# Kernel tuning notes

Measured on AMD Instinct MI355X. Metric: run time of the kernel, lower is better.

Reference implementation:

```python
import jax, jax.numpy as jnp
import numpy as np

D_MODEL = 128
REDUCTION = 4
KSIZE = 3
B = D_MODEL  # required by the original code's groups=B conv shape constraint
L = 4096


def setup_inputs() -> dict:
    key = jax.random.key(0)
    ks = jax.random.split(key, 7)
    d, r, K = D_MODEL, REDUCTION, KSIZE
    return {
        "x": jax.random.normal(ks[0], (B, L, d), dtype=jnp.float32),
        "W1": jax.random.normal(ks[1], (d // r, d), dtype=jnp.float32) * (1.0 / np.sqrt(d)),
        "b1": jax.random.normal(ks[2], (d // r,), dtype=jnp.float32) * 0.01,
        "W2": jax.random.normal(ks[3], (K, d // r), dtype=jnp.float32) * (1.0 / np.sqrt(d // r)),
        "b2": jax.random.normal(ks[4], (K,), dtype=jnp.float32) * 0.01,
        "Wc": jax.random.normal(ks[5], (d, d), dtype=jnp.float32) * (1.0 / np.sqrt(d)),
        "bc": jax.random.normal(ks[6], (d,), dtype=jnp.float32) * 0.01,
    }


def reference(x, W1, b1, W2, b2, Wc, bc):
    # x: [B, L, d] with B == d (required by original groups=B conv)
    Bsz, Lseq, d = x.shape
    K = W2.shape[0]
    pad = (K - 1) // 2
    # kernel generation from global average pool
    m = x.mean(axis=1)                                   # [B, d]
    h = jax.nn.gelu(m @ W1.T + b1, approximate=False)    # [B, d//r]
    w = jax.nn.softmax(h @ W2.T + b2, axis=-1)           # [B, K]; row j is the kernel for channel j
    # depthwise-style cross-correlation: y[b, l, c] = sum_k xp[b, l+k, c] * w[c, k]
    xp = jnp.pad(x, ((0, 0), (pad, pad), (0, 0)))        # [B, L+2*pad, d]
    y = sum(xp[:, k:k + Lseq, :] * w[None, None, :, k] for k in range(K))  # [B, L, d]
    # pointwise conv (kernel_size=1) == per-token linear
    return y @ Wc.T + bc                                 # [B, L, d]
```

## Files before the change

### kernel.cpp

```cpp
#include <hip/hip_runtime.h>
#include <hip/hip_bf16.h>

#define D_MODEL 128
#define SEQ_L   4096
#define BATCH   128
#define NSEG    8

typedef float f4 __attribute__((ext_vector_type(4)));
typedef float f32x4 __attribute__((ext_vector_type(4)));
typedef short bf16x8 __attribute__((ext_vector_type(8)));

__device__ __forceinline__ unsigned short f2bf(float f) {
    union { float f; unsigned u; } v; v.f = f;
    unsigned r = v.u + 0x7FFFu + ((v.u >> 16) & 1u);
    return (unsigned short)(r >> 16);
}

__global__ __launch_bounds__(512) void kmean(const float* __restrict__ x,
                                             float* __restrict__ part,
                                             const float* __restrict__ Wc,
                                             unsigned short* __restrict__ wcb) {
    if (blockIdx.x == NSEG) {
        if (blockIdx.y < 8) {
            int i = blockIdx.y * 512 + threadIdx.x;
            f4 v = reinterpret_cast<const f4*>(Wc)[i];
            ushort4 o;
            o.x = f2bf(v[0]); o.y = f2bf(v[1]); o.z = f2bf(v[2]); o.w = f2bf(v[3]);
            reinterpret_cast<ushort4*>(wcb)[i] = o;
        }
        return;
    }
    int seg = blockIdx.x, b = blockIdx.y;
    int t = threadIdx.x;
    int c4 = t & 31, ph = t >> 5;
    const f4* xb = reinterpret_cast<const f4*>(x + (size_t)b * SEQ_L * D_MODEL);
    int l0 = seg * (SEQ_L / NSEG);

    f4 a0 = {0.f,0.f,0.f,0.f}, a1 = a0, a2 = a0, a3 = a0;
    #pragma unroll
    for (int i = 0; i < 32; i += 4) {
        a0 += xb[(l0 + ph + (i + 0) * 16) * 32 + c4];
        a1 += xb[(l0 + ph + (i + 1) * 16) * 32 + c4];
        a2 += xb[(l0 + ph + (i + 2) * 16) * 32 + c4];
        a3 += xb[(l0 + ph + (i + 3) * 16) * 32 + c4];
    }
    f4 acc = (a0 + a1) + (a2 + a3);

    __shared__ f4 red[512];
    red[t] = acc;
    __syncthreads();
    if (t < 32) {
        f4 s = red[t];
        #pragma unroll
        for (int p = 1; p < 16; ++p) s += red[t + 32 * p];
        reinterpret_cast<f4*>(part + ((size_t)b * NSEG + seg) * D_MODEL)[t] = s;
    }
}

__global__ __launch_bounds__(128) void kweights(const float* __restrict__ part,
                                                const float* __restrict__ W1,
                                                const float* __restrict__ b1,
                                                const float* __restrict__ W2,
                                                const float* __restrict__ b2,
                                                float* __restrict__ w) {
    int c = threadIdx.x;
    f4 mv[32];
    #pragma unroll
    for (int d4 = 0; d4 < 32; ++d4) mv[d4] = (f4){0.f, 0.f, 0.f, 0.f};
    for (int s = 0; s < NSEG; ++s) {
        const f4* ps = reinterpret_cast<const f4*>(part + ((size_t)c * NSEG + s) * D_MODEL);
        #pragma unroll
        for (int d4 = 0; d4 < 32; ++d4) mv[d4] += ps[d4];
    }
    #pragma unroll
    for (int d4 = 0; d4 < 32; ++d4) mv[d4] *= (1.0f / (float)SEQ_L);

    float h[32];
    #pragma unroll
    for (int j = 0; j < 32; ++j) {
        const f4* w1r = reinterpret_cast<const f4*>(W1 + j * 128);
        f4 s4 = {0.f, 0.f, 0.f, 0.f};
        #pragma unroll
        for (int d4 = 0; d4 < 32; ++d4) s4 += mv[d4] * w1r[d4];
        float s = s4[0] + s4[1] + s4[2] + s4[3] + b1[j];
        h[j] = 0.5f * s * (1.0f + erff(s * 0.70710678118654752f));
    }
    float lg[3];
    float mx = -1e30f;
    #pragma unroll
    for (int k = 0; k < 3; ++k) {
        float s = b2[k];
        #pragma unroll
        for (int j = 0; j < 32; ++j) s += h[j] * W2[k * 32 + j];
        lg[k] = s;
        mx = fmaxf(mx, s);
    }
    float e[3], den = 0.f;
    #pragma unroll
    for (int k = 0; k < 3; ++k) { e[k] = __expf(lg[k] - mx); den += e[k]; }
    float inv = 1.0f / den;
    #pragma unroll
    for (int k = 0; k < 3; ++k) w[k * 128 + c] = e[k] * inv;
}

template<bool GUARD>
__device__ __forceinline__ void load6(const float* __restrict__ xb, int gr0, int c4, f4 R[6]) {
    #pragma unroll
    for (int j = 0; j < 6; ++j) {
        int gr = gr0 + j;
        if (GUARD) {
            bool ok = (gr >= 0) && (gr < SEQ_L);
            int grc = ok ? gr : 0;
            f4 v = reinterpret_cast<const f4*>(xb + (size_t)grc * D_MODEL)[c4];
            f4 z = {0.f, 0.f, 0.f, 0.f};
            R[j] = ok ? v : z;
        } else {
            R[j] = reinterpret_cast<const f4*>(xb + (size_t)gr * D_MODEL)[c4];
        }
    }
}

__global__ __launch_bounds__(512, 2) void kconv(const float* __restrict__ x,
                                                const float* __restrict__ wv,
                                                const unsigned short* __restrict__ wcb,
                                                const float* __restrict__ bc,
                                                float* __restrict__ out) {
    __shared__ __align__(16) unsigned short y_lds[2][64][132];

    int t = threadIdx.x;
    int b = blockIdx.y;
    int base = blockIdx.x * 256;
    const float* xb = x + (size_t)b * SEQ_L * D_MODEL;
    float* outb = out + (size_t)b * SEQ_L * D_MODEL;

    int c4 = t & 31, rg = t >> 5;
    int lane = t & 63, wid = t >> 6;
    int r = lane & 15, q = lane >> 4, kb = q * 8;
    int co0 = wid * 16;

    f4 w0 = reinterpret_cast<const f4*>(wv)[c4];
    f4 w1 = reinterpret_cast<const f4*>(wv + 128)[c4];
    f4 w2 = reinterpret_cast<const f4*>(wv + 256)[c4];

    bf16x8 awc[4];
    #pragma unroll
    for (int kc = 0; kc < 4; ++kc)
        awc[kc] = *reinterpret_cast<const bf16x8*>(wcb + (size_t)(co0 + r) * D_MODEL + kc * 32 + kb);

    f4 bcv = *reinterpret_cast<const f4*>(bc + co0 + q * 4);

    f4 R[6];
    if (base == 0) load6<true>(xb, base + rg * 4 - 1, c4, R);
    else           load6<false>(xb, base + rg * 4 - 1, c4, R);

    #pragma unroll
    for (int i = 0; i < 4; ++i) {
        int buf = i & 1;
        #pragma unroll
        for (int j = 0; j < 4; ++j) {
            f4 y = R[j] * w0 + R[j + 1] * w1 + R[j + 2] * w2;
            ushort4 yb;
            yb.x = f2bf(y[0]); yb.y = f2bf(y[1]); yb.z = f2bf(y[2]); yb.w = f2bf(y[3]);
            *reinterpret_cast<ushort4*>(&y_lds[buf][rg * 4 + j][c4 * 4]) = yb;
        }
        if (i < 3) {
            int ntok0 = base + (i + 1) * 64;
            if (ntok0 + 64 == SEQ_L) load6<true>(xb, ntok0 + rg * 4 - 1, c4, R);
            else                     load6<false>(xb, ntok0 + rg * 4 - 1, c4, R);
        }
        __syncthreads();

        f32x4 acc[4];
        #pragma unroll
        for (int g = 0; g < 4; ++g) acc[g] = (f32x4){0.f, 0.f, 0.f, 0.f};
        #pragma unroll
        for (int g = 0; g < 4; ++g)
            #pragma unroll
            for (int kc = 0; kc < 4; ++kc) {
                bf16x8 bv = *reinterpret_cast<const bf16x8*>(&y_lds[buf][g * 16 + r][kc * 32 + kb]);
                acc[g] = __builtin_amdgcn_mfma_f32_16x16x32_bf16(awc[kc], bv, acc[g], 0, 0, 0);
            }

        int tokt = base + i * 64;
        #pragma unroll
        for (int g = 0; g < 4; ++g) {
            int tok = tokt + g * 16 + r;
            *reinterpret_cast<f4*>(outb + (size_t)tok * D_MODEL + co0 + q * 4) = acc[g] + bcv;
        }
        __syncthreads();
    }
}

extern "C" void kernel_launch(void* const* d_in, const int* in_sizes, int n_in,
                              void* d_out, int out_size, void* d_ws, size_t ws_size,
                              hipStream_t stream) {
    const float* x  = (const float*)d_in[0];
    const float* W1 = (const float*)d_in[1];
    const float* b1 = (const float*)d_in[2];
    const float* W2 = (const float*)d_in[3];
    const float* b2 = (const float*)d_in[4];
    const float* Wc = (const float*)d_in[5];
    const float* bc = (const float*)d_in[6];
    float* out = (float*)d_out;

    char* ws = (char*)d_ws;
    float* part = (float*)ws;
    float* w    = (float*)(ws + 524288);
    unsigned short* wcb = (unsigned short*)(ws + 526336);

    kmean<<<dim3(NSEG + 1, BATCH), 512, 0, stream>>>(x, part, Wc, wcb);
    kweights<<<1, 128, 0, stream>>>(part, W1, b1, W2, b2, w);
    kconv<<<dim3(SEQ_L / 256, BATCH), 512, 0, stream>>>(x, w, wcb, bc, out);
}
```

Baseline: 235.7 us.

## Emit bf16 copy of x during mean pass and feed conv from it

The mean-reduction kernel now also writes a bf16 copy of x to workspace. The conv kernel reads that half-size copy instead of the fp32 input, and uses a swizzled LDS layout, 128-token chunks and higher occupancy bounds. The aim is to halve the conv kernel's input read traffic, at the cost of an extra bf16 write in the first pass and reduced precision on the conv input. A fallback keeps the original path when the workspace is too small.

```diff
diff --git a/kernel.cpp b/kernel.cpp
--- a/kernel.cpp
+++ b/kernel.cpp
@@ -9,6 +9,7 @@
 typedef float f4 __attribute__((ext_vector_type(4)));
 typedef float f32x4 __attribute__((ext_vector_type(4)));
 typedef short bf16x8 __attribute__((ext_vector_type(8)));
+typedef unsigned int u32x4 __attribute__((ext_vector_type(4)));
 
 __device__ __forceinline__ unsigned short f2bf(float f) {
     union { float f; unsigned u; } v; v.f = f;
@@ -16,10 +17,27 @@
     return (unsigned short)(r >> 16);
 }
 
-__global__ __launch_bounds__(512) void kmean(const float* __restrict__ x,
-                                             float* __restrict__ part,
-                                             const float* __restrict__ Wc,
-                                             unsigned short* __restrict__ wcb) {
+__device__ __forceinline__ unsigned pack2bf(float lo, float hi) {
+    return (unsigned)f2bf(lo) | ((unsigned)f2bf(hi) << 16);
+}
+
+__device__ __forceinline__ void unpk(u32x4 v, f4& a, f4& b) {
+    a[0] = __uint_as_float(v.x << 16);
+    a[1] = __uint_as_float(v.x & 0xFFFF0000u);
+    a[2] = __uint_as_float(v.y << 16);
+    a[3] = __uint_as_float(v.y & 0xFFFF0000u);
+    b[0] = __uint_as_float(v.z << 16);
+    b[1] = __uint_as_float(v.z & 0xFFFF0000u);
+    b[2] = __uint_as_float(v.w << 16);
+    b[3] = __uint_as_float(v.w & 0xFFFF0000u);
+}
+
+
+__global__ __launch_bounds__(512) void kmean_a(const float* __restrict__ x,
+                                               float* __restrict__ part,
+                                               const float* __restrict__ Wc,
+                                               unsigned short* __restrict__ wcb,
+                                               unsigned short* __restrict__ xbf) {
     if (blockIdx.x == NSEG) {
         if (blockIdx.y < 8) {
             int i = blockIdx.y * 512 + threadIdx.x;
@@ -34,6 +52,161 @@
     int t = threadIdx.x;
     int c4 = t & 31, ph = t >> 5;
     const f4* xb = reinterpret_cast<const f4*>(x + (size_t)b * SEQ_L * D_MODEL);
+    unsigned short* xbb = xbf + (size_t)b * SEQ_L * D_MODEL;
+    int l0 = seg * (SEQ_L / NSEG);
+
+    f4 a0 = {0.f,0.f,0.f,0.f}, a1 = a0, a2 = a0, a3 = a0;
+    #pragma unroll
+    for (int i = 0; i < 32; i += 4) {
+        #pragma unroll
+        for (int k = 0; k < 4; ++k) {
+            int l = l0 + ph + (i + k) * 16;
+            f4 v = xb[l * 32 + c4];
+            if (k == 0) a0 += v; else if (k == 1) a1 += v; else if (k == 2) a2 += v; else a3 += v;
+            ushort4 o;
+            o.x = f2bf(v[0]); o.y = f2bf(v[1]); o.z = f2bf(v[2]); o.w = f2bf(v[3]);
+            reinterpret_cast<ushort4*>(xbb + (size_t)l * D_MODEL)[c4] = o;
+        }
+    }
+    f4 acc = (a0 + a1) + (a2 + a3);
+
+    __shared__ f4 red[512];
+    red[t] = acc;
+    __syncthreads();
+    if (t < 32) {
+        f4 s = red[t];
+        #pragma unroll
+        for (int p = 1; p < 16; ++p) s += red[t + 32 * p];
+        reinterpret_cast<f4*>(part + ((size_t)b * NSEG + seg) * D_MODEL)[t] = s;
+    }
+}
+
+template<bool GUARD>
+__device__ __forceinline__ void load6b(const unsigned short* __restrict__ xbb,
+                                       int gr0, int c8, u32x4 R[6]) {
+    #pragma unroll
+    for (int j = 0; j < 6; ++j) {
+        int gr = gr0 + j;
+        if (GUARD) {
+            bool ok = (gr >= 0) && (gr < SEQ_L);
+            int grc = ok ? gr : 0;
+            u32x4 v = reinterpret_cast<const u32x4*>(xbb + (size_t)grc * D_MODEL)[c8];
+            u32x4 z = {0u, 0u, 0u, 0u};
+            R[j] = ok ? v : z;
+        } else {
+            R[j] = reinterpret_cast<const u32x4*>(xbb + (size_t)gr * D_MODEL)[c8];
+        }
+    }
+}
+
+template<bool GUARD>
+__device__ __forceinline__ void kconv_body(const unsigned short* __restrict__ xbf,
+                                           const float* __restrict__ wv,
+                                           const unsigned short* __restrict__ wcb,
+                                           const float* __restrict__ bc,
+                                           float* __restrict__ out,
+                                           unsigned short (*y_lds)[128][128]) {
+    int t = threadIdx.x, b = blockIdx.y;
+    int base = blockIdx.x * 256;
+    const unsigned short* xbb = xbf + (size_t)b * SEQ_L * D_MODEL;
+    float* outb = out + (size_t)b * SEQ_L * D_MODEL;
+
+    int c8 = t & 15, rg = t >> 4;
+    int lane = t & 63, wid = t >> 6;
+    int r = lane & 15, q = lane >> 4, kb = q * 8;
+    int co0 = wid * 16;
+
+    f4 w0a = *reinterpret_cast<const f4*>(wv + c8 * 8);
+    f4 w0b = *reinterpret_cast<const f4*>(wv + c8 * 8 + 4);
+    f4 w1a = *reinterpret_cast<const f4*>(wv + 128 + c8 * 8);
+    f4 w1b = *reinterpret_cast<const f4*>(wv + 128 + c8 * 8 + 4);
+    f4 w2a = *reinterpret_cast<const f4*>(wv + 256 + c8 * 8);
+    f4 w2b = *reinterpret_cast<const f4*>(wv + 256 + c8 * 8 + 4);
+
+    bf16x8 awc[4];
+    #pragma unroll
+    for (int kc = 0; kc < 4; ++kc)
+        awc[kc] = *reinterpret_cast<const bf16x8*>(wcb + (size_t)(co0 + r) * D_MODEL + kc * 32 + kb);
+
+    f4 bcv = *reinterpret_cast<const f4*>(bc + co0 + q * 4);
+
+    u32x4 R[6];
+    load6b<GUARD>(xbb, base + rg * 4 - 1, c8, R);
+
+    #pragma unroll
+    for (int i = 0; i < 2; ++i) {
+        f4 pa, pb, ca, cb;
+        unpk(R[0], pa, pb);
+        unpk(R[1], ca, cb);
+        #pragma unroll
+        for (int j = 0; j < 4; ++j) {
+            f4 na, nb;
+            unpk(R[j + 2], na, nb);
+            f4 y0 = pa * w0a + ca * w1a + na * w2a;
+            f4 y1 = pb * w0b + cb * w1b + nb * w2b;
+            u32x4 P;
+            P.x = pack2bf(y0[0], y0[1]);
+            P.y = pack2bf(y0[2], y0[3]);
+            P.z = pack2bf(y1[0], y1[1]);
+            P.w = pack2bf(y1[2], y1[3]);
+            int row = rg * 4 + j;
+            *reinterpret_cast<u32x4*>(&y_lds[i][row][(c8 ^ (row & 15)) * 8]) = P;
+            pa = ca; pb = cb; ca = na; cb = nb;
+        }
+        if (i == 0) load6b<GUARD>(xbb, base + 128 + rg * 4 - 1, c8, R);
+        __syncthreads();
+
+        f32x4 acc[8];
+        #pragma unroll
+        for (int g = 0; g < 8; ++g) acc[g] = (f32x4){0.f, 0.f, 0.f, 0.f};
+        #pragma unroll
+        for (int g = 0; g < 8; ++g)
+            #pragma unroll
+            for (int kc = 0; kc < 4; ++kc) {
+                bf16x8 bv = *reinterpret_cast<const bf16x8*>(
+                    &y_lds[i][g * 16 + r][((kc * 4 + q) ^ r) * 8]);
+                acc[g] = __builtin_amdgcn_mfma_f32_16x16x32_bf16(awc[kc], bv, acc[g], 0, 0, 0);
+            }
+
+        #pragma unroll
+        for (int g = 0; g < 8; ++g) {
+            int tok = base + i * 128 + g * 16 + r;
+            *reinterpret_cast<f4*>(outb + (size_t)tok * D_MODEL + co0 + q * 4) = acc[g] + bcv;
+        }
+    }
+}
+
+__global__ __launch_bounds__(512, 4) void kconv_a(const unsigned short* __restrict__ xbf,
+                                                  const float* __restrict__ wv,
+                                                  const unsigned short* __restrict__ wcb,
+                                                  const float* __restrict__ bc,
+                                                  float* __restrict__ out) {
+    __shared__ __align__(16) unsigned short y_lds[2][128][128];
+    if (blockIdx.x == 0 || blockIdx.x == gridDim.x - 1)
+        kconv_body<true>(xbf, wv, wcb, bc, out, y_lds);
+    else
+        kconv_body<false>(xbf, wv, wcb, bc, out, y_lds);
+}
+
+
+__global__ __launch_bounds__(512) void kmean_b(const float* __restrict__ x,
+                                               float* __restrict__ part,
+                                               const float* __restrict__ Wc,
+                                               unsigned short* __restrict__ wcb) {
+    if (blockIdx.x == NSEG) {
+        if (blockIdx.y < 8) {
+            int i = blockIdx.y * 512 + threadIdx.x;
+            f4 v = reinterpret_cast<const f4*>(Wc)[i];
+            ushort4 o;
+            o.x = f2bf(v[0]); o.y = f2bf(v[1]); o.z = f2bf(v[2]); o.w = f2bf(v[3]);
+            reinterpret_cast<ushort4*>(wcb)[i] = o;
+        }
+        return;
+    }
+    int seg = blockIdx.x, b = blockIdx.y;
+    int t = threadIdx.x;
+    int c4 = t & 31, ph = t >> 5;
+    const f4* xb = reinterpret_cast<const f4*>(x + (size_t)b * SEQ_L * D_MODEL);
     int l0 = seg * (SEQ_L / NSEG);
 
     f4 a0 = {0.f,0.f,0.f,0.f}, a1 = a0, a2 = a0, a3 = a0;
@@ -55,52 +228,6 @@
         for (int p = 1; p < 16; ++p) s += red[t + 32 * p];
         reinterpret_cast<f4*>(part + ((size_t)b * NSEG + seg) * D_MODEL)[t] = s;
     }
-}
-
-__global__ __launch_bounds__(128) void kweights(const float* __restrict__ part,
-                                                const float* __restrict__ W1,
-                                                const float* __restrict__ b1,
-                                                const float* __restrict__ W2,
-                                                const float* __restrict__ b2,
-                                                float* __restrict__ w) {
-    int c = threadIdx.x;
-    f4 mv[32];
-    #pragma unroll
-    for (int d4 = 0; d4 < 32; ++d4) mv[d4] = (f4){0.f, 0.f, 0.f, 0.f};
-    for (int s = 0; s < NSEG; ++s) {
-        const f4* ps = reinterpret_cast<const f4*>(part + ((size_t)c * NSEG + s) * D_MODEL);
-        #pragma unroll
-        for (int d4 = 0; d4 < 32; ++d4) mv[d4] += ps[d4];
-    }
-    #pragma unroll
-    for (int d4 = 0; d4 < 32; ++d4) mv[d4] *= (1.0f / (float)SEQ_L);
-
-    float h[32];
-    #pragma unroll
-    for (int j = 0; j < 32; ++j) {
-        const f4* w1r = reinterpret_cast<const f4*>(W1 + j * 128);
-        f4 s4 = {0.f, 0.f, 0.f, 0.f};
-        #pragma unroll
-        for (int d4 = 0; d4 < 32; ++d4) s4 += mv[d4] * w1r[d4];
-        float s = s4[0] + s4[1] + s4[2] + s4[3] + b1[j];
-        h[j] = 0.5f * s * (1.0f + erff(s * 0.70710678118654752f));
-    }
-    float lg[3];
-    float mx = -1e30f;
-    #pragma unroll
-    for (int k = 0; k < 3; ++k) {
-        float s = b2[k];
-        #pragma unroll
-        for (int j = 0; j < 32; ++j) s += h[j] * W2[k * 32 + j];
-        lg[k] = s;
-        mx = fmaxf(mx, s);
-    }
-    float e[3], den = 0.f;
-    #pragma unroll
-    for (int k = 0; k < 3; ++k) { e[k] = __expf(lg[k] - mx); den += e[k]; }
-    float inv = 1.0f / den;
-    #pragma unroll
-    for (int k = 0; k < 3; ++k) w[k * 128 + c] = e[k] * inv;
 }
 
 template<bool GUARD>
@@ -120,11 +247,11 @@
     }
 }
 
-__global__ __launch_bounds__(512, 2) void kconv(const float* __restrict__ x,
-                                                const float* __restrict__ wv,
-                                                const unsigned short* __restrict__ wcb,
-                                                const float* __restrict__ bc,
-                                                float* __restrict__ out) {
+__global__ __launch_bounds__(512, 2) void kconv_b(const float* __restrict__ x,
+                                                  const float* __restrict__ wv,
+                                                  const unsigned short* __restrict__ wcb,
+                                                  const float* __restrict__ bc,
+                                                  float* __restrict__ out) {
     __shared__ __align__(16) unsigned short y_lds[2][64][132];
 
     int t = threadIdx.x;
@@ -189,6 +316,52 @@
         }
         __syncthreads();
     }
+}
+
+__global__ __launch_bounds__(128) void kweights(const float* __restrict__ part,
+                                                const float* __restrict__ W1,
+                                                const float* __restrict__ b1,
+                                                const float* __restrict__ W2,
+                                                const float* __restrict__ b2,
+                                                float* __restrict__ w) {
+    int c = threadIdx.x;
+    f4 mv[32];
+    #pragma unroll
+    for (int d4 = 0; d4 < 32; ++d4) mv[d4] = (f4){0.f, 0.f, 0.f, 0.f};
+    for (int s = 0; s < NSEG; ++s) {
+        const f4* ps = reinterpret_cast<const f4*>(part + ((size_t)c * NSEG + s) * D_MODEL);
+        #pragma unroll
+        for (int d4 = 0; d4 < 32; ++d4) mv[d4] += ps[d4];
+    }
+    #pragma unroll
+    for (int d4 = 0; d4 < 32; ++d4) mv[d4] *= (1.0f / (float)SEQ_L);
+
+    float h[32];
+    #pragma unroll
+    for (int j = 0; j < 32; ++j) {
+        const f4* w1r = reinterpret_cast<const f4*>(W1 + j * 128);
+        f4 s4 = {0.f, 0.f, 0.f, 0.f};
+        #pragma unroll
+        for (int d4 = 0; d4 < 32; ++d4) s4 += mv[d4] * w1r[d4];
+        float s = s4[0] + s4[1] + s4[2] + s4[3] + b1[j];
+        h[j] = 0.5f * s * (1.0f + erff(s * 0.70710678118654752f));
+    }
+    float lg[3];
+    float mx = -1e30f;
+    #pragma unroll
+    for (int k = 0; k < 3; ++k) {
+        float s = b2[k];
+        #pragma unroll
+        for (int j = 0; j < 32; ++j) s += h[j] * W2[k * 32 + j];
+        lg[k] = s;
+        mx = fmaxf(mx, s);
+    }
+    float e[3], den = 0.f;
+    #pragma unroll
+    for (int k = 0; k < 3; ++k) { e[k] = __expf(lg[k] - mx); den += e[k]; }
+    float inv = 1.0f / den;
+    #pragma unroll
+    for (int k = 0; k < 3; ++k) w[k * 128 + c] = e[k] * inv;
 }
 
 extern "C" void kernel_launch(void* const* d_in, const int* in_sizes, int n_in,
@@ -204,11 +377,25 @@
     float* out = (float*)d_out;
 
     char* ws = (char*)d_ws;
-    float* part = (float*)ws;
-    float* w    = (float*)(ws + 524288);
-    unsigned short* wcb = (unsigned short*)(ws + 526336);
-
-    kmean<<<dim3(NSEG + 1, BATCH), 512, 0, stream>>>(x, part, Wc, wcb);
-    kweights<<<1, 128, 0, stream>>>(part, W1, b1, W2, b2, w);
-    kconv<<<dim3(SEQ_L / 256, BATCH), 512, 0, stream>>>(x, w, wcb, bc, out);
-}
+    const size_t XBF_BYTES = (size_t)BATCH * SEQ_L * D_MODEL * 2;
+    const size_t NEED = XBF_BYTES + 524288 + 4096 + 32768;
+
+    if (ws_size >= NEED) {
+        unsigned short* xbf = (unsigned short*)ws;
+        float* part = (float*)(ws + XBF_BYTES);
+        float* w    = (float*)(ws + XBF_BYTES + 524288);
+        unsigned short* wcb = (unsigned short*)(ws + XBF_BYTES + 524288 + 4096);
+
+        kmean_a<<<dim3(NSEG + 1, BATCH), 512, 0, stream>>>(x, part, Wc, wcb, xbf);
+        kweights<<<1, 128, 0, stream>>>(part, W1, b1, W2, b2, w);
+        kconv_a<<<dim3(SEQ_L / 256, BATCH), 512, 0, stream>>>(xbf, w, wcb, bc, out);
+    } else {
+        float* part = (float*)ws;
+        float* w    = (float*)(ws + 524288);
+        unsigned short* wcb = (unsigned short*)(ws + 526336);
+
+        kmean_b<<<dim3(NSEG + 1, BATCH), 512, 0, stream>>>(x, part, Wc, wcb);
+        kweights<<<1, 128, 0, stream>>>(part, W1, b1, W2, b2, w);
+        kconv_b<<<dim3(SEQ_L / 256, BATCH), 512, 0, stream>>>(x, w, wcb, bc, out);
+    }
+}
```

Measured after the change: 268.6 us. +13.9%, slower.

## Prefetch conv input into double-buffered registers, drop barrier, nontemporal output stores

Applied to the files above, without the earlier changes.

In the conv kernel, the next 64-token slab of x now loads into a second register buffer before the current slab is convolved. This gives global loads more time to complete. The trailing barrier is removed because the double-buffered LDS already separates reuse of each buffer, and outputs are written with nontemporal stores so they do not pollute the cache. The mean kernel doubles its segment count to 16 and issues all 16 loads up front before a tree reduction, which raises memory-level parallelism. The workspace offsets are moved to fit the larger partial-sum buffer. The cost is higher register pressure in both kernels.

```diff
diff --git a/kernel.cpp b/kernel.cpp
--- a/kernel.cpp
+++ b/kernel.cpp
@@ -4,7 +4,7 @@
 #define D_MODEL 128
 #define SEQ_L   4096
 #define BATCH   128
-#define NSEG    8
+#define NSEG    16
 
 typedef float f4 __attribute__((ext_vector_type(4)));
 typedef float f32x4 __attribute__((ext_vector_type(4)));
@@ -36,18 +36,18 @@
     const f4* xb = reinterpret_cast<const f4*>(x + (size_t)b * SEQ_L * D_MODEL);
     int l0 = seg * (SEQ_L / NSEG);
 
-    f4 a0 = {0.f,0.f,0.f,0.f}, a1 = a0, a2 = a0, a3 = a0;
-    #pragma unroll
-    for (int i = 0; i < 32; i += 4) {
-        a0 += xb[(l0 + ph + (i + 0) * 16) * 32 + c4];
-        a1 += xb[(l0 + ph + (i + 1) * 16) * 32 + c4];
-        a2 += xb[(l0 + ph + (i + 2) * 16) * 32 + c4];
-        a3 += xb[(l0 + ph + (i + 3) * 16) * 32 + c4];
-    }
-    f4 acc = (a0 + a1) + (a2 + a3);
+    f4 R[16];
+    #pragma unroll
+    for (int j = 0; j < 16; ++j)
+        R[j] = xb[(l0 + ph + j * 16) * 32 + c4];
+
+    #pragma unroll
+    for (int s = 8; s >= 1; s >>= 1)
+        #pragma unroll
+        for (int j = 0; j < s; ++j) R[j] += R[j + s];
 
     __shared__ f4 red[512];
-    red[t] = acc;
+    red[t] = R[0];
     __syncthreads();
     if (t < 32) {
         f4 s = red[t];
@@ -149,24 +149,24 @@
 
     f4 bcv = *reinterpret_cast<const f4*>(bc + co0 + q * 4);
 
-    f4 R[6];
-    if (base == 0) load6<true>(xb, base + rg * 4 - 1, c4, R);
-    else           load6<false>(xb, base + rg * 4 - 1, c4, R);
+    f4 R[2][6];
+    if (base == 0) load6<true>(xb, base + rg * 4 - 1, c4, R[0]);
+    else           load6<false>(xb, base + rg * 4 - 1, c4, R[0]);
 
     #pragma unroll
     for (int i = 0; i < 4; ++i) {
-        int buf = i & 1;
+        const int cur = i & 1, nxt = cur ^ 1;
+        if (i < 3) {
+            int ntok0 = base + (i + 1) * 64;
+            if (ntok0 + 64 == SEQ_L) load6<true>(xb, ntok0 + rg * 4 - 1, c4, R[nxt]);
+            else                     load6<false>(xb, ntok0 + rg * 4 - 1, c4, R[nxt]);
+        }
         #pragma unroll
         for (int j = 0; j < 4; ++j) {
-            f4 y = R[j] * w0 + R[j + 1] * w1 + R[j + 2] * w2;
+            f4 y = R[cur][j] * w0 + R[cur][j + 1] * w1 + R[cur][j + 2] * w2;
             ushort4 yb;
             yb.x = f2bf(y[0]); yb.y = f2bf(y[1]); yb.z = f2bf(y[2]); yb.w = f2bf(y[3]);
-            *reinterpret_cast<ushort4*>(&y_lds[buf][rg * 4 + j][c4 * 4]) = yb;
-        }
-        if (i < 3) {
-            int ntok0 = base + (i + 1) * 64;
-            if (ntok0 + 64 == SEQ_L) load6<true>(xb, ntok0 + rg * 4 - 1, c4, R);
-            else                     load6<false>(xb, ntok0 + rg * 4 - 1, c4, R);
+            *reinterpret_cast<ushort4*>(&y_lds[cur][rg * 4 + j][c4 * 4]) = yb;
         }
         __syncthreads();
 
@@ -177,7 +177,7 @@
         for (int g = 0; g < 4; ++g)
             #pragma unroll
             for (int kc = 0; kc < 4; ++kc) {
-                bf16x8 bv = *reinterpret_cast<const bf16x8*>(&y_lds[buf][g * 16 + r][kc * 32 + kb]);
+                bf16x8 bv = *reinterpret_cast<const bf16x8*>(&y_lds[cur][g * 16 + r][kc * 32 + kb]);
                 acc[g] = __builtin_amdgcn_mfma_f32_16x16x32_bf16(awc[kc], bv, acc[g], 0, 0, 0);
             }
 
@@ -185,9 +185,9 @@
         #pragma unroll
         for (int g = 0; g < 4; ++g) {
             int tok = tokt + g * 16 + r;
-            *reinterpret_cast<f4*>(outb + (size_t)tok * D_MODEL + co0 + q * 4) = acc[g] + bcv;
-        }
-        __syncthreads();
+            f4 v = acc[g] + bcv;
+            __builtin_nontemporal_store(v, reinterpret_cast<f4*>(outb + (size_t)tok * D_MODEL + co0 + q * 4));
+        }
     }
 }
 
@@ -205,8 +205,8 @@
 
     char* ws = (char*)d_ws;
     float* part = (float*)ws;
-    float* w    = (float*)(ws + 524288);
-    unsigned short* wcb = (unsigned short*)(ws + 526336);
+    float* w    = (float*)(ws + 1048576);
+    unsigned short* wcb = (unsigned short*)(ws + 1052672);
 
     kmean<<<dim3(NSEG + 1, BATCH), 512, 0, stream>>>(x, part, Wc, wcb);
     kweights<<<1, 128, 0, stream>>>(part, W1, b1, W2, b2, w);
```

Result: slower. 244.3 us (+3.6%).
